# Kernel tuning notes

Measured on AMD Instinct MI355X. Metric: run time of the kernel, lower is better.

The kernel has to match this reference:

```python
import jax, jax.numpy as jnp
import numpy as np

B, C, H, W = 32, 256, 60, 60
E, O, K = 3, 256, 3          # num_experts, out_channels, kernel_size
SQ = 16                      # squeeze_channels = max(C//16, 16)
PAD, STRIDE = 1, 1
DN = ('NCHW', 'OIHW', 'NCHW')

# ---- bicubic 3->5 interpolation matrix (PyTorch bicubic, a=-0.75, align_corners=False) ----
def _cubic(t, a=-0.75):
    t = abs(t)
    if t <= 1.0:
        return (a + 2) * t**3 - (a + 3) * t**2 + 1
    if t < 2.0:
        return a * t**3 - 5 * a * t**2 + 8 * a * t - 4 * a
    return 0.0

def _bicubic_mat(n_in=3, n_out=5):
    M = np.zeros((n_out, n_in), np.float32)
    s = n_in / n_out
    for o in range(n_out):
        x = (o + 0.5) * s - 0.5
        x0 = int(np.floor(x)); f = x - x0
        for j in range(-1, 3):  # 4-tap cubic, indices clamped (border replicate)
            M[o, min(max(x0 + j, 0), n_in - 1)] += _cubic(f - j)
    return M

BICUBIC_M = jnp.asarray(_bicubic_mat())

def _pool(x, k):
    # exact PyTorch AdaptiveAvgPool2d when H,W divisible by k (true for H=W=60)
    b, c, h, w = x.shape
    return x.reshape(b, c, k, h // k, k, w // k).mean((3, 5))

def _conv(x, w, groups=1, pad=0, stride=1):
    return jax.lax.conv_general_dilated(x, w, (stride, stride), [(pad, pad)] * 2,
                                         dimension_numbers=DN, feature_group_count=groups)

def setup_inputs() -> dict:
    key = jax.random.key(0)
    ks = jax.random.split(key, 6)
    x = jax.random.normal(ks[0], (B, C, H, W), jnp.float32)
    w_expert = jax.random.normal(ks[1], (E, O, C, K, K), jnp.float32) / np.sqrt(C * K * K)
    rw1  = jax.random.normal(ks[2], (SQ, 3 * C, 1, 1), jnp.float32) / np.sqrt(3 * C)
    rdw1 = jax.random.normal(ks[3], (SQ, 1, 3, 3), jnp.float32) / 3.0
    rdw2 = jax.random.normal(ks[4], (SQ, 1, 3, 3), jnp.float32) / 3.0
    rw2  = jax.random.normal(ks[5], (E * C, SQ, 1, 1), jnp.float32) / np.sqrt(SQ)
    return {"x": x, "w_expert": w_expert, "rw1": rw1, "rdw1": rdw1, "rdw2": rdw2, "rw2": rw2}

def reference(x, w_expert, rw1, rdw1, rdw2, rw2):
    b = x.shape[0]
    # --- routing function (mode 'A') ---
    a1 = jnp.broadcast_to(_pool(x, 1), (b, C, 5, 5))          # gap1 expanded to 5x5
    p3 = _pool(x, 3)
    M = BICUBIC_M
    a3 = jnp.einsum('oi,bcij,pj->bcop', M, p3, M)             # bicubic 3x3 -> 5x5
    a5 = _pool(x, 5)
    att = jnp.concatenate([a1, a3, a5], axis=1)               # (b, 3C, 5, 5)
    h = jax.nn.relu(_conv(att, rw1))                          # (b, SQ, 5, 5)
    h = jax.nn.relu(_conv(h, rdw1, groups=SQ))                # (b, SQ, 3, 3)
    h = jax.nn.relu(_conv(h, rdw2, groups=SQ))                # (b, SQ, 1, 1)
    r = jax.nn.sigmoid(_conv(h, rw2)).reshape(b, E, C)        # (b, E, C)
    # --- combine expert kernels per sample, apply per-sample conv ---
    cw = jnp.einsum('bec,eockl->bockl', r, w_expert)          # (b, O, C, K, K)
    y = jax.vmap(lambda xi, wi: _conv(xi[None], wi, pad=PAD, stride=STRIDE)[0])(x, cw)
    return y
```

## Files before the change

### kernel.cpp

```cpp
#include <hip/hip_runtime.h>

typedef unsigned short u16;
typedef unsigned int u32;
typedef __attribute__((ext_vector_type(8))) short bfrag;
typedef __attribute__((ext_vector_type(4))) float facc;

#define GAS __attribute__((address_space(1)))
#define LAS __attribute__((address_space(3)))

__device__ __forceinline__ u16 f2bf(float f) {
  u32 u = __builtin_bit_cast(u32, f);
  u = (u + 0x7fffu + ((u >> 16) & 1u)) >> 16;
  return (u16)u;
}
__device__ __forceinline__ float bf2f(u16 b) {
  u32 u = ((u32)b) << 16;
  return __builtin_bit_cast(float, u);
}

__device__ __forceinline__ void glds16(const u16* src, u16* dst) {
  __builtin_amdgcn_global_load_lds((const GAS unsigned int*)src,
                                   (LAS unsigned int*)dst, 16, 0, 0);
}

__device__ __constant__ float Mb[5][3] = {
  { 1.096f, -0.096f,  0.0f  },
  { 0.612f,  0.46f,  -0.072f},
  { 0.0f,    1.0f,    0.0f  },
  {-0.072f,  0.46f,   0.612f},
  { 0.0f,   -0.096f,  1.096f},
};

__global__ __launch_bounds__(256) void att_kernel(const float* __restrict__ x,
                                                  float* __restrict__ att) {
  int bc = blockIdx.x;
  int b = bc >> 8, c = bc & 255;
  const float* xc = x + (size_t)bc * 3600;
  __shared__ float s15[225];
  __shared__ float p3s[9];
  int t = threadIdx.x;
  if (t < 225) {
    int i = t / 15, j = t - (t / 15) * 15;
    const float* base = xc + i * 4 * 60 + j * 4;
    float s = 0.f;
#pragma unroll
    for (int r = 0; r < 4; ++r) {
      float4 v = *reinterpret_cast<const float4*>(base + r * 60);
      s += v.x + v.y + v.z + v.w;
    }
    s15[t] = s;
  }
  __syncthreads();
  float a5v = 0.f;
  if (t < 25) {
    int ii = t / 5, jj = t - (t / 5) * 5;
    float s = 0.f;
#pragma unroll
    for (int r = 0; r < 3; ++r)
#pragma unroll
      for (int cc = 0; cc < 3; ++cc) s += s15[(ii * 3 + r) * 15 + jj * 3 + cc];
    a5v = s * (1.f / 144.f);
  }
  if (t >= 64 && t < 73) {
    int i3 = t - 64;
    int pi = i3 / 3, pj = i3 - pi * 3;
    float s = 0.f;
#pragma unroll
    for (int r = 0; r < 5; ++r)
#pragma unroll
      for (int cc = 0; cc < 5; ++cc) s += s15[(pi * 5 + r) * 15 + pj * 5 + cc];
    p3s[i3] = s * (1.f / 400.f);
  }
  __syncthreads();
  float* attb = att + (size_t)b * 768 * 25;
  if (t < 25) {
    attb[(512 + c) * 25 + t] = a5v;
    int o = t / 5, qq = t - (t / 5) * 5;
    float s = 0.f;
#pragma unroll
    for (int i = 0; i < 3; ++i) {
      float mi = Mb[o][i];
#pragma unroll
      for (int j = 0; j < 3; ++j) s += mi * Mb[qq][j] * p3s[i * 3 + j];
    }
    attb[(256 + c) * 25 + t] = s;
  } else if (t == 32) {
    float s = 0.f;
#pragma unroll
    for (int i = 0; i < 9; ++i) s += p3s[i];
    s *= (1.f / 9.f);
    for (int p = 0; p < 25; ++p) attb[c * 25 + p] = s;
  }
}

__global__ __launch_bounds__(256) void route_kernel(
    const float* __restrict__ att, const float* __restrict__ rw1,
    const float* __restrict__ rdw1, const float* __restrict__ rdw2,
    const float* __restrict__ rw2, float* __restrict__ rout) {
  int b = blockIdx.x;
  int t = threadIdx.x;
  __shared__ u16 attS[768 * 25];
  __shared__ float h1[16 * 25];
  __shared__ float h2[16 * 9];
  __shared__ float h3[16];
  const float* attb = att + (size_t)b * 768 * 25;
  for (int i = t; i < 768 * 25; i += 256) attS[i] = f2bf(attb[i]);
  __syncthreads();
  for (int idx = t; idx < 400; idx += 256) {
    int sq = idx / 25, p = idx - (idx / 25) * 25;
    const float* wrow = rw1 + sq * 768;
    float s = 0.f;
    for (int ic = 0; ic < 768; ++ic) s += wrow[ic] * bf2f(attS[ic * 25 + p]);
    h1[idx] = fmaxf(s, 0.f);
  }
  __syncthreads();
  for (int idx = t; idx < 144; idx += 256) {
    int sq = idx / 9, ij = idx - (idx / 9) * 9;
    int i = ij / 3, j = ij - (ij / 3) * 3;
    float s = 0.f;
#pragma unroll
    for (int u = 0; u < 3; ++u)
#pragma unroll
      for (int v = 0; v < 3; ++v)
        s += rdw1[sq * 9 + u * 3 + v] * h1[sq * 25 + (i + u) * 5 + (j + v)];
    h2[idx] = fmaxf(s, 0.f);
  }
  __syncthreads();
  if (t < 16) {
    float s = 0.f;
#pragma unroll
    for (int uv = 0; uv < 9; ++uv) s += rdw2[t * 9 + uv] * h2[t * 9 + uv];
    h3[t] = fmaxf(s, 0.f);
  }
  __syncthreads();
  for (int idx = t; idx < 768; idx += 256) {
    float s = 0.f;
#pragma unroll
    for (int sq = 0; sq < 16; ++sq) s += rw2[idx * 16 + sq] * h3[sq];
    rout[(size_t)b * 768 + idx] = 1.f / (1.f + expf(-s));
  }
}

__global__ __launch_bounds__(256) void cw_kernel(const float* __restrict__ rout,
                                                 const float* __restrict__ we,
                                                 u16* __restrict__ cw) {
  int idx = blockIdx.x * 256 + threadIdx.x;
  if (idx >= 32 * 256 * 256) return;
  int b = idx >> 16;
  int oc = idx & 65535;
  int o = oc >> 8, c = oc & 255;
  float r0 = rout[b * 768 + c];
  float r1 = rout[b * 768 + 256 + c];
  float r2 = rout[b * 768 + 512 + c];
  const size_t ES = (size_t)256 * 256 * 9;
  const float* w0 = we + ((size_t)o * 256 + c) * 9;
  int ctile = c >> 6, c_loc = c & 63;
  u16* dst = cw + ((size_t)(b * 256 + o)) * 2304 + ctile * 576 + c_loc;
#pragma unroll
  for (int tp = 0; tp < 9; ++tp) {
    float f = r0 * w0[tp] + r1 * w0[ES + tp] + r2 * w0[2 * ES + tp];
    dst[tp * 64] = f2bf(f);
  }
}

__global__ __launch_bounds__(256) void xprep_kernel(const float* __restrict__ x,
                                                    u16* __restrict__ xpad) {
  const int row = blockIdx.x;
  const int b = blockIdx.y;
  const int t = threadIdx.x;
  u16* outrow = xpad + ((size_t)(b * 62 + row)) * 64 * 256;
  if (row == 0 || row == 61) {
    uint4 z = {0, 0, 0, 0};
#pragma unroll
    for (int i = 0; i < 8; ++i)
      *reinterpret_cast<uint4*>(outrow + (size_t)(t + i * 256) * 8) = z;
    return;
  }
  const int h = row - 1;
  __shared__ float xs[64 * 62];
  const float* xb = x + ((size_t)b * 256) * 3600 + h * 60;
  for (int cc = 0; cc < 4; ++cc) {
    for (int u = t; u < 960; u += 256) {
      int c = u / 15, seg = u - (u / 15) * 15;
      float4 v = *reinterpret_cast<const float4*>(xb + (size_t)(cc * 64 + c) * 3600 + seg * 4);
      float* d = &xs[c * 62 + seg * 4];
      d[0] = v.x; d[1] = v.y; d[2] = v.z; d[3] = v.w;
    }
    __syncthreads();
    for (int u = t; u < 512; u += 256) {
      int col = u >> 3, slot = u & 7;
      uint4 o = {0, 0, 0, 0};
      if (col >= 1 && col <= 60) {
        int w = col - 1;
        u16 tmp[8];
#pragma unroll
        for (int j = 0; j < 8; ++j) tmp[j] = f2bf(xs[(slot * 8 + j) * 62 + w]);
        o = *reinterpret_cast<uint4*>(tmp);
      }
      *reinterpret_cast<uint4*>(outrow + (size_t)col * 256 + cc * 64 + slot * 8) = o;
    }
    __syncthreads();
  }
}

__global__ __launch_bounds__(256, 2) void conv_kernel(const u16* __restrict__ xpad,
                                                      const u16* __restrict__ cw,
                                                      float* __restrict__ y) {
  __shared__ __align__(16) u16 smem[32768];

  const int flat = blockIdx.x;
  const int wg = (flat & 7) * 240 + (flat >> 3);
  const int b = wg / 60;
  const int r2 = wg - b * 60;
  const int ot = r2 / 30, rp = r2 - (r2 / 30) * 30;
  const int o0 = ot * 128, h0 = rp * 2;

  const int t = threadIdx.x;
  const int wave = t >> 6, lane = t & 63;
  const int wm = wave >> 1, wn = wave & 1;
  const int q = lane >> 4, r16 = lane & 15, l7 = lane & 7;

  const u16* cwB = cw + (size_t)(b * 256 + o0) * 2304;
  const u16* xpB = xpad + ((size_t)(b * 62 + h0) * 64) * 256;

  int a_src[4], a_du[4];
#pragma unroll
  for (int i = 0; i < 4; ++i) {
    int u = wave * 256 + i * 64 + lane;
    int m = u >> 3, sd = u & 7, ss = sd ^ (m & 7);
    a_src[i] = m * 2304 + ss * 8;
    a_du[i] = u * 8;
  }
  int x_src[8], x_du[8];
#pragma unroll
  for (int i = 0; i < 8; ++i) {
    int u = wave * 512 + i * 64 + lane;
    int row = u >> 9, col = (u >> 3) & 63, sd = u & 7, ss = sd ^ (col & 7);
    x_src[i] = (row * 64 + col) * 256 + ss * 8;
    x_du[i] = u * 8;
  }

  const int abase = (wm * 64 + r16) * 64;
  const int aq = (q ^ l7) * 8;
  int bct[3];
#pragma unroll
  for (int kw = 0; kw < 3; ++kw) {
    int rk = r16 + kw;
    bct[kw] = rk * 64 + ((q ^ (rk & 7)) * 8);
  }

  facc acc[4][4] = {};

  auto stageA = [&](int koff, int bufsel) {
    u16* dst = smem + 16384 + bufsel * 8192;
#pragma unroll
    for (int i = 0; i < 4; ++i) glds16(cwB + a_src[i] + koff, dst + a_du[i]);
  };
  auto stageX = [&](int ct) {
#pragma unroll
    for (int i = 0; i < 8; ++i) glds16(xpB + x_src[i] + ct * 64, smem + x_du[i]);
  };

  stageX(0);
  stageA(0, 0);
  __syncthreads();

  for (int ct = 0; ct < 4; ++ct) {
#pragma unroll
    for (int tap = 0; tap < 9; ++tap) {
      const int cur = (ct + tap) & 1;
      const bool last = (ct == 3 && tap == 8);
      if (!last) stageA((ct * 9 + tap + 1) * 64, cur ^ 1);
      {
        const int kh = tap / 3, kw = tap % 3;
        const u16* Ab = smem + 16384 + cur * 8192;
        const int bbase = (wn + kh) * 4096 + bct[kw];
#pragma unroll
        for (int ks = 0; ks < 2; ++ks) {
          const int kx = ks * 32;
          bfrag a[4], bb[4];
#pragma unroll
          for (int mf = 0; mf < 4; ++mf)
            a[mf] = *reinterpret_cast<const bfrag*>(Ab + ((abase + mf * 1024 + aq) ^ kx));
#pragma unroll
          for (int nf = 0; nf < 4; ++nf)
            bb[nf] = *reinterpret_cast<const bfrag*>(smem + ((bbase + nf * 1024) ^ kx));
#pragma unroll
          for (int mf = 0; mf < 4; ++mf)
#pragma unroll
            for (int nf = 0; nf < 4; ++nf)
              acc[mf][nf] = __builtin_amdgcn_mfma_f32_16x16x32_bf16(a[mf], bb[nf], acc[mf][nf], 0, 0, 0);
        }
      }
      __syncthreads();
      if (tap == 8 && ct < 3) { stageX(ct + 1); __syncthreads(); }
    }
  }

  float* yB = y + (size_t)(b * 256 + o0 + wm * 64) * 3600 + (size_t)(h0 + wn) * 60;
#pragma unroll
  for (int mf = 0; mf < 4; ++mf)
#pragma unroll
    for (int nf = 0; nf < 4; ++nf) {
      int w = nf * 16 + r16;
      if (w < 60) {
#pragma unroll
        for (int rr = 0; rr < 4; ++rr) {
          int o_loc = mf * 16 + q * 4 + rr;
          yB[(size_t)o_loc * 3600 + w] = acc[mf][nf][rr];
        }
      }
    }
}

extern "C" void kernel_launch(void* const* d_in, const int* in_sizes, int n_in,
                              void* d_out, int out_size, void* d_ws, size_t ws_size,
                              hipStream_t stream) {
  const float* x    = (const float*)d_in[0];
  const float* we   = (const float*)d_in[1];
  const float* rw1  = (const float*)d_in[2];
  const float* rdw1 = (const float*)d_in[3];
  const float* rdw2 = (const float*)d_in[4];
  const float* rw2  = (const float*)d_in[5];
  float* y = (float*)d_out;

  char* ws = (char*)d_ws;
  float* att  = (float*)ws;
  float* rout = (float*)(ws + 2457600);
  u16*   cwp  = (u16*)(ws + 2555904);
  u16*   xpad = (u16*)(ws + 40304640);

  xprep_kernel<<<dim3(62, 32), 256, 0, stream>>>(x, xpad);
  att_kernel<<<8192, 256, 0, stream>>>(x, att);
  route_kernel<<<32, 256, 0, stream>>>(att, rw1, rdw1, rdw2, rw2, rout);
  cw_kernel<<<8192, 256, 0, stream>>>(rout, we, cwp);
  conv_kernel<<<1920, 256, 0, stream>>>(xpad, cwp, y);
  (void)in_sizes; (void)n_in; (void)out_size; (void)ws_size;
}
```

Measured before the change: 244.7 us.

## Enlarge conv tile to all 256 outputs x 4 rows using 32x32 MFMA

The per-sample conv kernel now has each 512-thread workgroup compute all 256 output channels for 4 output rows, instead of 128 channels for 2 rows. It switches from 16x16x32 to 32x32x16 bf16 MFMA with 16-float accumulators, and shrinks the grid from 1920 to 480 blocks. The larger tile reuses each staged x tile across all output channels and each weight tile across more rows, which cuts global and LDS traffic per FLOP. In exchange it uses about 112KB of LDS per block, more registers, and fewer blocks, which may lower occupancy and leave a partial last wave across the CUs.

```diff
diff --git a/kernel.cpp b/kernel.cpp
--- a/kernel.cpp
+++ b/kernel.cpp
@@ -3,7 +3,7 @@
 typedef unsigned short u16;
 typedef unsigned int u32;
 typedef __attribute__((ext_vector_type(8))) short bfrag;
-typedef __attribute__((ext_vector_type(4))) float facc;
+typedef __attribute__((ext_vector_type(16))) float f32x16;
 
 #define GAS __attribute__((address_space(1)))
 #define LAS __attribute__((address_space(3)))
@@ -203,62 +203,60 @@
   }
 }
 
-__global__ __launch_bounds__(256, 2) void conv_kernel(const u16* __restrict__ xpad,
+__global__ __launch_bounds__(512, 2) void conv_kernel(const u16* __restrict__ xpad,
                                                       const u16* __restrict__ cw,
                                                       float* __restrict__ y) {
-  __shared__ __align__(16) u16 smem[32768];
+  __shared__ __align__(16) u16 smem[57344];
 
   const int flat = blockIdx.x;
-  const int wg = (flat & 7) * 240 + (flat >> 3);
-  const int b = wg / 60;
-  const int r2 = wg - b * 60;
-  const int ot = r2 / 30, rp = r2 - (r2 / 30) * 30;
-  const int o0 = ot * 128, h0 = rp * 2;
+  const int wg = (flat & 7) * 60 + (flat >> 3);
+  const int b = wg / 15;
+  const int rg = wg - b * 15;
+  const int h0 = rg * 4;
 
   const int t = threadIdx.x;
   const int wave = t >> 6, lane = t & 63;
-  const int wm = wave >> 1, wn = wave & 1;
-  const int q = lane >> 4, r16 = lane & 15, l7 = lane & 7;
-
-  const u16* cwB = cw + (size_t)(b * 256 + o0) * 2304;
+  const int wm = wave >> 2, wn = wave & 3;
+  const int r32 = lane & 31, half = lane >> 5, l7 = lane & 7;
+
+  const u16* cwB = cw + (size_t)b * 256 * 2304;
   const u16* xpB = xpad + ((size_t)(b * 62 + h0) * 64) * 256;
 
   int a_src[4], a_du[4];
 #pragma unroll
   for (int i = 0; i < 4; ++i) {
-    int u = wave * 256 + i * 64 + lane;
+    int u = i * 512 + t;
     int m = u >> 3, sd = u & 7, ss = sd ^ (m & 7);
     a_src[i] = m * 2304 + ss * 8;
     a_du[i] = u * 8;
   }
-  int x_src[8], x_du[8];
-#pragma unroll
-  for (int i = 0; i < 8; ++i) {
-    int u = wave * 512 + i * 64 + lane;
+  int x_src[6], x_du[6];
+#pragma unroll
+  for (int i = 0; i < 6; ++i) {
+    int u = i * 512 + t;
     int row = u >> 9, col = (u >> 3) & 63, sd = u & 7, ss = sd ^ (col & 7);
     x_src[i] = (row * 64 + col) * 256 + ss * 8;
     x_du[i] = u * 8;
   }
 
-  const int abase = (wm * 64 + r16) * 64;
-  const int aq = (q ^ l7) * 8;
-  int bct[3];
+  const int abase = wm * 8192 + r32 * 64 + ((half ^ l7) * 8);
+  int bcb[3];
 #pragma unroll
   for (int kw = 0; kw < 3; ++kw) {
-    int rk = r16 + kw;
-    bct[kw] = rk * 64 + ((q ^ (rk & 7)) * 8);
-  }
-
-  facc acc[4][4] = {};
+    int rk = r32 + kw;
+    bcb[kw] = rk * 64 + ((half ^ (rk & 7)) * 8);
+  }
+
+  f32x16 acc[4][2] = {};
 
   auto stageA = [&](int koff, int bufsel) {
-    u16* dst = smem + 16384 + bufsel * 8192;
+    u16* dst = smem + 24576 + bufsel * 16384;
 #pragma unroll
     for (int i = 0; i < 4; ++i) glds16(cwB + a_src[i] + koff, dst + a_du[i]);
   };
   auto stageX = [&](int ct) {
 #pragma unroll
-    for (int i = 0; i < 8; ++i) glds16(xpB + x_src[i] + ct * 64, smem + x_du[i]);
+    for (int i = 0; i < 6; ++i) glds16(xpB + x_src[i] + ct * 64, smem + x_du[i]);
   };
 
   stageX(0);
@@ -268,28 +266,28 @@
   for (int ct = 0; ct < 4; ++ct) {
 #pragma unroll
     for (int tap = 0; tap < 9; ++tap) {
-      const int cur = (ct + tap) & 1;
+      const int cur = (ct * 9 + tap) & 1;
       const bool last = (ct == 3 && tap == 8);
       if (!last) stageA((ct * 9 + tap + 1) * 64, cur ^ 1);
       {
-        const int kh = tap / 3, kw = tap % 3;
-        const u16* Ab = smem + 16384 + cur * 8192;
-        const int bbase = (wn + kh) * 4096 + bct[kw];
-#pragma unroll
-        for (int ks = 0; ks < 2; ++ks) {
-          const int kx = ks * 32;
-          bfrag a[4], bb[4];
+        const int kh = tap / 3, kw = tap - kh * 3;
+        const u16* Ab = smem + 24576 + cur * 16384;
+        const int bb_base = (wn + kh) * 4096 + bcb[kw];
+#pragma unroll
+        for (int kg = 0; kg < 4; ++kg) {
+          const int kx = kg << 4;
+          bfrag a[4], bb[2];
 #pragma unroll
           for (int mf = 0; mf < 4; ++mf)
-            a[mf] = *reinterpret_cast<const bfrag*>(Ab + ((abase + mf * 1024 + aq) ^ kx));
-#pragma unroll
-          for (int nf = 0; nf < 4; ++nf)
-            bb[nf] = *reinterpret_cast<const bfrag*>(smem + ((bbase + nf * 1024) ^ kx));
+            a[mf] = *reinterpret_cast<const bfrag*>(Ab + ((abase + mf * 2048) ^ kx));
+#pragma unroll
+          for (int nf = 0; nf < 2; ++nf)
+            bb[nf] = *reinterpret_cast<const bfrag*>(smem + ((bb_base + nf * 2048) ^ kx));
 #pragma unroll
           for (int mf = 0; mf < 4; ++mf)
 #pragma unroll
-            for (int nf = 0; nf < 4; ++nf)
-              acc[mf][nf] = __builtin_amdgcn_mfma_f32_16x16x32_bf16(a[mf], bb[nf], acc[mf][nf], 0, 0, 0);
+            for (int nf = 0; nf < 2; ++nf)
+              acc[mf][nf] = __builtin_amdgcn_mfma_f32_32x32x16_bf16(a[mf], bb[nf], acc[mf][nf], 0, 0, 0);
         }
       }
       __syncthreads();
@@ -297,18 +295,20 @@
     }
   }
 
-  float* yB = y + (size_t)(b * 256 + o0 + wm * 64) * 3600 + (size_t)(h0 + wn) * 60;
+  float* yB = y + ((size_t)(b * 256 + wm * 128)) * 3600 + (size_t)(h0 + wn) * 60;
 #pragma unroll
   for (int mf = 0; mf < 4; ++mf)
 #pragma unroll
-    for (int nf = 0; nf < 4; ++nf) {
-      int w = nf * 16 + r16;
+    for (int nf = 0; nf < 2; ++nf) {
+      int w = nf * 32 + r32;
       if (w < 60) {
 #pragma unroll
-        for (int rr = 0; rr < 4; ++rr) {
-          int o_loc = mf * 16 + q * 4 + rr;
-          yB[(size_t)o_loc * 3600 + w] = acc[mf][nf][rr];
-        }
+        for (int g = 0; g < 4; ++g)
+#pragma unroll
+          for (int rr = 0; rr < 4; ++rr) {
+            int o_loc = mf * 32 + g * 8 + half * 4 + rr;
+            yB[(size_t)o_loc * 3600 + w] = acc[mf][nf][g * 4 + rr];
+          }
       }
     }
 }
@@ -334,6 +334,6 @@
   att_kernel<<<8192, 256, 0, stream>>>(x, att);
   route_kernel<<<32, 256, 0, stream>>>(att, rw1, rdw1, rdw2, rw2, rout);
   cw_kernel<<<8192, 256, 0, stream>>>(rout, we, cwp);
-  conv_kernel<<<1920, 256, 0, stream>>>(xpad, cwp, y);
+  conv_kernel<<<480, 512, 0, stream>>>(xpad, cwp, y);
   (void)in_sizes; (void)n_in; (void)out_size; (void)ws_size;
 }
```

Result: slower. 250.6 us (+2.4%).
